# Kernel optimization log

Measured on AMD Instinct MI355X. Metric: run time of the kernel, lower is better.

The kernel has to match this reference:

```python
import jax, jax.numpy as jnp
import numpy as np

B, S, D = 4, 4096, 2048      # batch, seq, model_dim
E = 128                      # emb_dim (hardcoded in module)
H = 128                      # head_dim
TAU = 0.4                    # self.T
BASE = 3.0                   # self.base (gumbel-sigmoid offset)
LN_EPS = 1e-5


def setup_inputs() -> dict:
    key = jax.random.key(0)
    k_x, k_wr, k_wd, k_g = jax.random.split(key, 4)
    x = jax.random.normal(k_x, (B, S, D), dtype=jnp.float32)
    # torch nn.Linear stores weight as [out_features, in_features]
    W_router = jax.random.normal(k_wr, (E, D), dtype=jnp.float32) / np.sqrt(D)
    W_decoder = jax.random.normal(k_wd, (H, E), dtype=jnp.float32) / np.sqrt(E)
    ln_gamma = jnp.ones((E,), dtype=jnp.float32)
    ln_beta = jnp.zeros((E,), dtype=jnp.float32)
    rnn_state = jnp.zeros((E,), dtype=jnp.float32)  # registered buffer, zeros
    # torch: gumbels = -Exp(1).log()  -> standard Gumbel(0,1) noise
    u = jax.random.uniform(k_g, (B, S, H), dtype=jnp.float32, minval=1e-20, maxval=1.0)
    gumbel_noise = -jnp.log(-jnp.log(u))
    return {
        "x": x, "W_router": W_router, "W_decoder": W_decoder,
        "ln_gamma": ln_gamma, "ln_beta": ln_beta, "rnn_state": rnn_state,
        "gumbel_noise": gumbel_noise, "top_k": 32,
    }


def reference(x, W_router, W_decoder, ln_gamma, ln_beta, rnn_state, gumbel_noise, top_k):
    # router linear (no bias): [B,S,D] @ [D,E] -> [B,S,E]
    out = jnp.einsum("bsd,ed->bse", x, W_router)
    full_emb = rnn_state + out
    # LayerNorm over emb dim (biased variance, as torch LayerNorm)
    mu = full_emb.mean(-1, keepdims=True)
    var = full_emb.var(-1, keepdims=True)
    h = (full_emb - mu) / jnp.sqrt(var + LN_EPS) * ln_gamma + ln_beta
    # decoder linear after exact GELU: [B,S,E] @ [E,H] -> [B,S,H]
    logits = jnp.einsum("bse,he->bsh", jax.nn.gelu(h, approximate=False), W_decoder)
    # gumbel-sigmoid (soft): sigmoid((logits + gumbel + offset)/tau)
    binary_approx = jax.nn.sigmoid((logits + gumbel_noise + BASE) / TAU)
    # hard_sample: straight-through round
    binary = jax.lax.stop_gradient(jnp.round(binary_approx) - binary_approx) + binary_approx
    # top-k mask over head_dim
    _, topk_idx = jax.lax.top_k(binary_approx, top_k)            # [B,S,top_k]
    topk_mask = jax.nn.one_hot(topk_idx, H, dtype=binary_approx.dtype).sum(-2)  # [B,S,H]
    cnt = binary.sum(-1, keepdims=True)
    binary = jnp.where(cnt > top_k, topk_mask, binary)
    # fallback: if a token selects nothing, pick argmax of soft scores
    zero_mask = binary.sum(-1, keepdims=True) == 0
    fallback = jax.nn.one_hot(jnp.argmax(binary_approx, axis=-1), H, dtype=binary_approx.dtype)
    binary = jnp.where(zero_mask, fallback, binary)
    binary = binary.reshape(B, S, -1, H)  # [B,S,1,H]
    return binary, binary_approx
```

## Files before the change

### kernel.cpp

```cpp
#include <hip/hip_runtime.h>
#include <math.h>

#define NTOK   16384
#define DDIM   2048
#define EDIM   128
#define HDIM   128
#define TOKT   64
#define KC     32
#define NIT    32

typedef __attribute__((ext_vector_type(8))) _Float16 half8;
typedef __attribute__((ext_vector_type(4))) float    f32x4;

__device__ __forceinline__ int swz(int t, int e) {
  return t * EDIM + ((e & 96) | ((e ^ t) & 31));
}

__device__ __forceinline__ void cvt8(const float4& a, const float4& b,
                                     half8& h, half8& l) {
#pragma unroll
  for (int m = 0; m < 4; ++m) {
    const float v = (&a.x)[m];
    const _Float16 hv = (_Float16)v;
    h[m] = hv; l[m] = (_Float16)((v - (float)hv) * 2048.0f);
  }
#pragma unroll
  for (int m = 0; m < 4; ++m) {
    const float v = (&b.x)[m];
    const _Float16 hv = (_Float16)v;
    h[m + 4] = hv; l[m + 4] = (_Float16)((v - (float)hv) * 2048.0f);
  }
}

__global__ __launch_bounds__(256)
void conv_w(const float* __restrict__ Wr,
            _Float16* __restrict__ wh, _Float16* __restrict__ wl) {
  const int idx  = (int)blockIdx.x * 256 + (int)threadIdx.x;
  const int lane = idx & 63;
  const int ks   = (idx >> 6) & 63;
  const int nt   = idx >> 12;
  const int n    = nt * 16 + (lane & 15);
  const int k0   = ks * 32 + (lane >> 4) * 8;
  half8 h, l;
#pragma unroll
  for (int j = 0; j < 8; ++j) {
    const float w = Wr[(size_t)n * DDIM + k0 + j] * 32.0f;
    const _Float16 hh = (_Float16)w;
    h[j] = hh;
    l[j] = (_Float16)((w - (float)hh) * 2048.0f);
  }
  *(half8*)(wh + (size_t)idx * 8) = h;
  *(half8*)(wl + (size_t)idx * 8) = l;
}

__global__ __launch_bounds__(512, 2)
void fused_router(const float* __restrict__ x,
                  const _Float16* __restrict__ wsh,
                  const _Float16* __restrict__ wsl,
                  const float* __restrict__ Wd,
                  const float* __restrict__ gamma,
                  const float* __restrict__ beta,
                  const float* __restrict__ rnn,
                  const float* __restrict__ gum,
                  float* __restrict__ outb,
                  float* __restrict__ outa) {
  __shared__ char smraw[65536];
  _Float16* const xs = (_Float16*)smraw;
  float* const A  = (float*)smraw;
  float* const G4 = (float*)(smraw + 32768);

  const int tid  = (int)threadIdx.x;
  const int wv   = __builtin_amdgcn_readfirstlane(tid >> 6);
  const int lane = tid & 63;
  const int t0   = (int)blockIdx.x * TOKT;

  const int mw   = wv & 1;
  const int nw   = (wv >> 1) & 1;
  const int kw   = wv >> 2;
  const int quad = lane >> 4;
  const int col  = lane & 15;

  const int abase = (kw * 4 + mw * 2) * 1024 + lane * 8;

  const int skw   = tid >> 8;
  const int smt   = (tid >> 6) & 3;
  const int slane = tid & 63;
  const int woff  = (skw * 4 + smt) * 1024 + slane * 8;
  const float* xg = x + (size_t)(t0 + smt * 16 + (slane & 15)) * DDIM
                      + skw * 1024 + (slane >> 4) * 8;

  const size_t wbase = (size_t)(nw * 4) * 32768 + (size_t)kw * 16384 + lane * 8;

  f32x4 hh[2][4], cr[2][4];
#pragma unroll
  for (int mi = 0; mi < 2; ++mi)
#pragma unroll
    for (int ni = 0; ni < 4; ++ni) { hh[mi][ni] = (f32x4){0,0,0,0}; cr[mi][ni] = (f32x4){0,0,0,0}; }

  half8 bh[2][4], bl[2][4];

#pragma unroll
  for (int j = 0; j < 4; ++j) {
    bh[0][j] = *(const half8*)(wsh + wbase + (size_t)j * 32768);
    bl[0][j] = *(const half8*)(wsl + wbase + (size_t)j * 32768);
  }
  {
    const float4 a  = *(const float4*)xg;
    const float4 b2 = *(const float4*)(xg + 4);
    half8 h, l; cvt8(a, b2, h, l);
    *(half8*)&xs[woff] = h;
    *(half8*)&xs[woff + 512] = l;
  }

  auto body = [&](int i, int pb) {
    __syncthreads();
    const int ab = pb ? 8192 + abase : abase;
    const half8 ah0 = *(const half8*)&xs[ab];
    const half8 al0 = *(const half8*)&xs[ab + 512];
    const half8 ah1 = *(const half8*)&xs[ab + 1024];
    const half8 al1 = *(const half8*)&xs[ab + 1536];
    const int np = pb ^ 1;
    float4 pxa, pxb;
    if (i + 1 < NIT) {
      const size_t wo = wbase + (size_t)(i + 1) * 512;
#pragma unroll
      for (int j = 0; j < 4; ++j) {
        bh[np][j] = *(const half8*)(wsh + wo + (size_t)j * 32768);
        bl[np][j] = *(const half8*)(wsl + wo + (size_t)j * 32768);
      }
      pxa = *(const float4*)(xg + (i + 1) * KC);
      pxb = *(const float4*)(xg + (i + 1) * KC + 4);
    }
#pragma unroll
    for (int j = 0; j < 4; ++j) {
      hh[0][j] = __builtin_amdgcn_mfma_f32_16x16x32_f16(ah0, bh[pb][j], hh[0][j], 0, 0, 0);
      cr[0][j] = __builtin_amdgcn_mfma_f32_16x16x32_f16(ah0, bl[pb][j], cr[0][j], 0, 0, 0);
      cr[0][j] = __builtin_amdgcn_mfma_f32_16x16x32_f16(al0, bh[pb][j], cr[0][j], 0, 0, 0);
      hh[1][j] = __builtin_amdgcn_mfma_f32_16x16x32_f16(ah1, bh[pb][j], hh[1][j], 0, 0, 0);
      cr[1][j] = __builtin_amdgcn_mfma_f32_16x16x32_f16(ah1, bl[pb][j], cr[1][j], 0, 0, 0);
      cr[1][j] = __builtin_amdgcn_mfma_f32_16x16x32_f16(al1, bh[pb][j], cr[1][j], 0, 0, 0);
    }
    if (i + 1 < NIT) {
      half8 h, l; cvt8(pxa, pxb, h, l);
      *(half8*)&xs[np * 8192 + woff] = h;
      *(half8*)&xs[np * 8192 + woff + 512] = l;
    }
  };
  for (int ii = 0; ii < NIT; ii += 2) { body(ii, 0); body(ii + 1, 1); }
  __syncthreads();

  if (kw == 0) {
#pragma unroll
    for (int mi = 0; mi < 2; ++mi)
#pragma unroll
      for (int ni = 0; ni < 4; ++ni)
#pragma unroll
        for (int r = 0; r < 4; ++r) {
          const int t = (mw * 2 + mi) * 16 + quad * 4 + r;
          const int e = (nw * 4 + ni) * 16 + col;
          A[swz(t, e)] = hh[mi][ni][r] * (1.0f / 32.0f)
                       + cr[mi][ni][r] * (1.0f / 65536.0f);
        }
  }
  __syncthreads();
  if (kw == 1) {
    float rv[4];
#pragma unroll
    for (int ni = 0; ni < 4; ++ni) rv[ni] = rnn[(nw * 4 + ni) * 16 + col];
#pragma unroll
    for (int mi = 0; mi < 2; ++mi)
#pragma unroll
      for (int ni = 0; ni < 4; ++ni)
#pragma unroll
        for (int r = 0; r < 4; ++r) {
          const int t = (mw * 2 + mi) * 16 + quad * 4 + r;
          const int e = (nw * 4 + ni) * 16 + col;
          A[swz(t, e)] += hh[mi][ni][r] * (1.0f / 32.0f)
                        + cr[mi][ni][r] * (1.0f / 65536.0f) + rv[ni];
        }
  }
  __syncthreads();

  {
    const float gm0 = gamma[lane], gm1 = gamma[lane + 64];
    const float bt0 = beta[lane],  bt1 = beta[lane + 64];
    for (int tt = wv * 8; tt < wv * 8 + 8; ++tt) {
      const float v0 = A[swz(tt, lane)];
      const float v1 = A[swz(tt, lane + 64)];
      float s = v0 + v1;
#pragma unroll
      for (int m = 32; m; m >>= 1) s += __shfl_xor(s, m);
      const float mu = s * (1.0f / 128.0f);
      const float d0 = v0 - mu, d1 = v1 - mu;
      float q = d0 * d0 + d1 * d1;
#pragma unroll
      for (int m = 32; m; m >>= 1) q += __shfl_xor(q, m);
      const float rstd = 1.0f / sqrtf(q * (1.0f / 128.0f) + 1e-5f);
      const float h0v = d0 * rstd * gm0 + bt0;
      const float h1v = d1 * rstd * gm1 + bt1;
      const float g0 = 0.5f * h0v * (1.0f + erff(h0v * 0.70710678118654752f));
      const float g1 = 0.5f * h1v * (1.0f + erff(h1v * 0.70710678118654752f));
      const int e0a = lane, e1a = lane + 64;
      G4[(tt * 32 + (((e0a >> 2) ^ (tt & 31)))) * 4 + (e0a & 3)] = g0;
      G4[(tt * 32 + (((e1a >> 2) ^ (tt & 31)))) * 4 + (e1a & 3)] = g1;
    }
  }
  __syncthreads();

  {
    const int rbase = wv * 16;
    float acc2[16];
#pragma unroll
    for (int j = 0; j < 16; ++j) acc2[j] = 0.0f;
    const float4* wd4 = (const float4*)(Wd + (size_t)rbase * EDIM);
#pragma unroll 2
    for (int kg = 0; kg < EDIM / 4; ++kg) {
      const float4 gv = *(const float4*)&G4[(lane * 32 + (kg ^ (lane & 31))) * 4];
#pragma unroll
      for (int j = 0; j < 16; ++j) {
        const float4 w = wd4[(size_t)j * (EDIM / 4) + kg];
        acc2[j] = fmaf(gv.x, w.x,
                  fmaf(gv.y, w.y,
                  fmaf(gv.z, w.z,
                  fmaf(gv.w, w.w, acc2[j]))));
      }
    }
#pragma unroll
    for (int j = 0; j < 16; ++j) A[swz(lane, rbase + j)] = acc2[j];
  }
  __syncthreads();

  for (int tt = wv * 8; tt < wv * 8 + 8; ++tt) {
    const size_t T = (size_t)(t0 + tt);
    const float l0 = A[swz(tt, lane)];
    const float l1 = A[swz(tt, lane + 64)];
    const float gn0 = gum[T * HDIM + lane];
    const float gn1 = gum[T * HDIM + lane + 64];
    const float z0 = (l0 + gn0 + 3.0f) * 2.5f;
    const float z1 = (l1 + gn1 + 3.0f) * 2.5f;
    const float ba0 = 1.0f / (1.0f + expf(-z0));
    const float ba1 = 1.0f / (1.0f + expf(-z1));
    const unsigned ub0 = __float_as_uint(ba0);
    const unsigned ub1 = __float_as_uint(ba1);
    const int r0 = ba0 > 0.5f;
    const int r1 = ba1 > 0.5f;
    const int cnt = __popcll(__ballot(r0)) + __popcll(__ballot(r1));
    float bin0, bin1;
    if (cnt > 32) {
      unsigned v = 0u;
#pragma unroll
      for (int b = 29; b >= 0; --b) {
        const unsigned cand = v | (1u << b);
        const int cc = __popcll(__ballot(ub0 >= cand)) + __popcll(__ballot(ub1 >= cand));
        if (cc >= 32) v = cand;
      }
      const int cgt = __popcll(__ballot(ub0 > v)) + __popcll(__ballot(ub1 > v));
      const int r = 32 - cgt;
      const unsigned long long t0b = __ballot(ub0 == v);
      const unsigned long long t1b = __ballot(ub1 == v);
      const int n0 = __popcll(t0b);
      const unsigned long long mlt = (1ull << lane) - 1ull;
      const int rk0 = __popcll(t0b & mlt);
      const int rk1 = n0 + __popcll(t1b & mlt);
      bin0 = (ub0 > v || (ub0 == v && rk0 < r)) ? 1.0f : 0.0f;
      bin1 = (ub1 > v || (ub1 == v && rk1 < r)) ? 1.0f : 0.0f;
    } else if (cnt == 0) {
      float m = fmaxf(ba0, ba1);
#pragma unroll
      for (int mm = 32; mm; mm >>= 1) m = fmaxf(m, __shfl_xor(m, mm));
      const unsigned long long e0b = __ballot(ba0 == m);
      const unsigned long long e1b = __ballot(ba1 == m);
      const int hstar = e0b ? (__ffsll((unsigned long long)e0b) - 1)
                            : (64 + __ffsll((unsigned long long)e1b) - 1);
      bin0 = (lane == hstar) ? 1.0f : 0.0f;
      bin1 = (lane + 64 == hstar) ? 1.0f : 0.0f;
    } else {
      bin0 = r0 ? 1.0f : 0.0f;
      bin1 = r1 ? 1.0f : 0.0f;
    }
    outb[T * HDIM + lane]      = bin0;
    outb[T * HDIM + lane + 64] = bin1;
    outa[T * HDIM + lane]      = ba0;
    outa[T * HDIM + lane + 64] = ba1;
  }
}

extern "C" void kernel_launch(void* const* d_in, const int* in_sizes, int n_in,
                              void* d_out, int out_size, void* d_ws, size_t ws_size,
                              hipStream_t stream) {
  (void)in_sizes; (void)n_in; (void)ws_size; (void)out_size;
  const float* x   = (const float*)d_in[0];
  const float* Wr  = (const float*)d_in[1];
  const float* Wd  = (const float*)d_in[2];
  const float* gm  = (const float*)d_in[3];
  const float* bt  = (const float*)d_in[4];
  const float* rnn = (const float*)d_in[5];
  const float* gum = (const float*)d_in[6];
  float* outb = (float*)d_out;
  float* outa = outb + (size_t)NTOK * HDIM;

  _Float16* wh = (_Float16*)d_ws;
  _Float16* wl = wh + (size_t)EDIM * DDIM;

  conv_w<<<dim3(128), dim3(256), 0, stream>>>(Wr, wh, wl);
  fused_router<<<dim3(NTOK / TOKT), dim3(512), 0, stream>>>(
      x, wh, wl, Wd, gm, bt, rnn, gum, outb, outa);
}
```

Baseline: 281.3 us.

## Switch router GEMM to 32x32x16 MFMA with full-K per wave and larger K rounds

Restructures the split-fp16 router GEMM to use 32x32x16 MFMA tiles. Each of 8 waves now owns one 32x32 output tile over the full K range, where before the waves split K in two and reduced through LDS. Each barrier round now stages 128 K-columns instead of 32, with an XOR-swizzled LDS layout, and the weight preconversion kernel is reordered to match the new fragment layout. This cuts barrier count and the cross-wave reduction, at the cost of longer per-wave MFMA chains and unbuffered weight loads from global memory inside the inner loop. A barrier is also added before the decoder results overwrite the shared buffer.

```diff
diff --git a/kernel.cpp b/kernel.cpp
--- a/kernel.cpp
+++ b/kernel.cpp
@@ -6,11 +6,14 @@
 #define EDIM   128
 #define HDIM   128
 #define TOKT   64
-#define KC     32
-#define NIT    32
-
-typedef __attribute__((ext_vector_type(8))) _Float16 half8;
-typedef __attribute__((ext_vector_type(4))) float    f32x4;
+#define NRND   16
+#define KRND   128
+
+typedef __attribute__((ext_vector_type(8)))  _Float16 half8;
+typedef __attribute__((ext_vector_type(4)))  float    f32x4;
+typedef __attribute__((ext_vector_type(16))) float    f32x16;
+
+#define MFMA32 __builtin_amdgcn_mfma_f32_32x32x16_f16
 
 __device__ __forceinline__ int swz(int t, int e) {
   return t * EDIM + ((e & 96) | ((e ^ t) & 31));
@@ -37,10 +40,10 @@
             _Float16* __restrict__ wh, _Float16* __restrict__ wl) {
   const int idx  = (int)blockIdx.x * 256 + (int)threadIdx.x;
   const int lane = idx & 63;
-  const int ks   = (idx >> 6) & 63;
-  const int nt   = idx >> 12;
-  const int n    = nt * 16 + (lane & 15);
-  const int k0   = ks * 32 + (lane >> 4) * 8;
+  const int ks   = (idx >> 6) & 127;
+  const int nt   = idx >> 13;
+  const int n    = nt * 32 + (lane & 31);
+  const int k0   = ks * 16 + (lane >> 5) * 8;
   half8 h, l;
 #pragma unroll
   for (int j = 0; j < 8; ++j) {
@@ -65,7 +68,7 @@
                   float* __restrict__ outb,
                   float* __restrict__ outa) {
   __shared__ char smraw[65536];
-  _Float16* const xs = (_Float16*)smraw;
+  char* const sm = smraw;
   float* const A  = (float*)smraw;
   float* const G4 = (float*)(smraw + 32768);
 
@@ -74,110 +77,85 @@
   const int lane = tid & 63;
   const int t0   = (int)blockIdx.x * TOKT;
 
-  const int mw   = wv & 1;
-  const int nw   = (wv >> 1) & 1;
-  const int kw   = wv >> 2;
-  const int quad = lane >> 4;
-  const int col  = lane & 15;
-
-  const int abase = (kw * 4 + mw * 2) * 1024 + lane * 8;
-
-  const int skw   = tid >> 8;
-  const int smt   = (tid >> 6) & 3;
-  const int slane = tid & 63;
-  const int woff  = (skw * 4 + smt) * 1024 + slane * 8;
-  const float* xg = x + (size_t)(t0 + smt * 16 + (slane & 15)) * DDIM
-                      + skw * 1024 + (slane >> 4) * 8;
-
-  const size_t wbase = (size_t)(nw * 4) * 32768 + (size_t)kw * 16384 + lane * 8;
-
-  f32x4 hh[2][4], cr[2][4];
-#pragma unroll
-  for (int mi = 0; mi < 2; ++mi)
-#pragma unroll
-    for (int ni = 0; ni < 4; ++ni) { hh[mi][ni] = (f32x4){0,0,0,0}; cr[mi][ni] = (f32x4){0,0,0,0}; }
-
-  half8 bh[2][4], bl[2][4];
-
-#pragma unroll
-  for (int j = 0; j < 4; ++j) {
-    bh[0][j] = *(const half8*)(wsh + wbase + (size_t)j * 32768);
-    bl[0][j] = *(const half8*)(wsl + wbase + (size_t)j * 32768);
-  }
-  {
-    const float4 a  = *(const float4*)xg;
-    const float4 b2 = *(const float4*)(xg + 4);
-    half8 h, l; cvt8(a, b2, h, l);
-    *(half8*)&xs[woff] = h;
-    *(half8*)&xs[woff + 512] = l;
-  }
-
-  auto body = [&](int i, int pb) {
+  const int mt = wv >> 2;
+  const int nt = wv & 3;
+
+  const int s_tok = (tid & 7) + ((tid >> 6) << 3);
+  const int s_s   = (tid >> 3) & 7;
+  const int s_row = s_tok & 31;
+  const int s_mt  = s_tok >> 5;
+  const float* xg = x + (size_t)(t0 + s_tok) * DDIM + s_s * 16;
+  const int wbase = (s_s * 2 + s_mt) * 2048;
+  const int widx0 = (((0 * 32 + s_row) ^ s_s) * 16);
+  const int widx1 = (((1 * 32 + s_row) ^ s_s) * 16);
+
+  const size_t wbf = (size_t)nt * 65536 + (size_t)lane * 8;
+
+  f32x16 hh, cr;
+#pragma unroll
+  for (int g = 0; g < 16; ++g) { hh[g] = 0.0f; cr[g] = 0.0f; }
+
+  {
+    const float4 a0 = *(const float4*)(xg + 0);
+    const float4 a1 = *(const float4*)(xg + 4);
+    const float4 a2 = *(const float4*)(xg + 8);
+    const float4 a3 = *(const float4*)(xg + 12);
+    half8 h0, l0, h1, l1;
+    cvt8(a0, a1, h0, l0);
+    cvt8(a2, a3, h1, l1);
+    char* dst = sm;
+    *(half8*)(dst + wbase + widx0)        = h0;
+    *(half8*)(dst + wbase + 1024 + widx0) = l0;
+    *(half8*)(dst + wbase + widx1)        = h1;
+    *(half8*)(dst + wbase + 1024 + widx1) = l1;
+  }
+
+  for (int r = 0; r < NRND; ++r) {
     __syncthreads();
-    const int ab = pb ? 8192 + abase : abase;
-    const half8 ah0 = *(const half8*)&xs[ab];
-    const half8 al0 = *(const half8*)&xs[ab + 512];
-    const half8 ah1 = *(const half8*)&xs[ab + 1024];
-    const half8 al1 = *(const half8*)&xs[ab + 1536];
-    const int np = pb ^ 1;
-    float4 pxa, pxb;
-    if (i + 1 < NIT) {
-      const size_t wo = wbase + (size_t)(i + 1) * 512;
-#pragma unroll
-      for (int j = 0; j < 4; ++j) {
-        bh[np][j] = *(const half8*)(wsh + wo + (size_t)j * 32768);
-        bl[np][j] = *(const half8*)(wsl + wo + (size_t)j * 32768);
-      }
-      pxa = *(const float4*)(xg + (i + 1) * KC);
-      pxb = *(const float4*)(xg + (i + 1) * KC + 4);
-    }
-#pragma unroll
-    for (int j = 0; j < 4; ++j) {
-      hh[0][j] = __builtin_amdgcn_mfma_f32_16x16x32_f16(ah0, bh[pb][j], hh[0][j], 0, 0, 0);
-      cr[0][j] = __builtin_amdgcn_mfma_f32_16x16x32_f16(ah0, bl[pb][j], cr[0][j], 0, 0, 0);
-      cr[0][j] = __builtin_amdgcn_mfma_f32_16x16x32_f16(al0, bh[pb][j], cr[0][j], 0, 0, 0);
-      hh[1][j] = __builtin_amdgcn_mfma_f32_16x16x32_f16(ah1, bh[pb][j], hh[1][j], 0, 0, 0);
-      cr[1][j] = __builtin_amdgcn_mfma_f32_16x16x32_f16(ah1, bl[pb][j], cr[1][j], 0, 0, 0);
-      cr[1][j] = __builtin_amdgcn_mfma_f32_16x16x32_f16(al1, bh[pb][j], cr[1][j], 0, 0, 0);
-    }
-    if (i + 1 < NIT) {
-      half8 h, l; cvt8(pxa, pxb, h, l);
-      *(half8*)&xs[np * 8192 + woff] = h;
-      *(half8*)&xs[np * 8192 + woff + 512] = l;
-    }
-  };
-  for (int ii = 0; ii < NIT; ii += 2) { body(ii, 0); body(ii + 1, 1); }
-  __syncthreads();
-
-  if (kw == 0) {
-#pragma unroll
-    for (int mi = 0; mi < 2; ++mi)
-#pragma unroll
-      for (int ni = 0; ni < 4; ++ni)
-#pragma unroll
-        for (int r = 0; r < 4; ++r) {
-          const int t = (mw * 2 + mi) * 16 + quad * 4 + r;
-          const int e = (nw * 4 + ni) * 16 + col;
-          A[swz(t, e)] = hh[mi][ni][r] * (1.0f / 32.0f)
-                       + cr[mi][ni][r] * (1.0f / 65536.0f);
-        }
-  }
-  __syncthreads();
-  if (kw == 1) {
-    float rv[4];
-#pragma unroll
-    for (int ni = 0; ni < 4; ++ni) rv[ni] = rnn[(nw * 4 + ni) * 16 + col];
-#pragma unroll
-    for (int mi = 0; mi < 2; ++mi)
-#pragma unroll
-      for (int ni = 0; ni < 4; ++ni)
-#pragma unroll
-        for (int r = 0; r < 4; ++r) {
-          const int t = (mw * 2 + mi) * 16 + quad * 4 + r;
-          const int e = (nw * 4 + ni) * 16 + col;
-          A[swz(t, e)] += hh[mi][ni][r] * (1.0f / 32.0f)
-                        + cr[mi][ni][r] * (1.0f / 65536.0f) + rv[ni];
-        }
+    float4 p0, p1, p2, p3;
+    if (r + 1 < NRND) {
+      const float* xn = xg + (r + 1) * KRND;
+      p0 = *(const float4*)(xn + 0);
+      p1 = *(const float4*)(xn + 4);
+      p2 = *(const float4*)(xn + 8);
+      p3 = *(const float4*)(xn + 12);
+    }
+    const char* bb = sm + (r & 1) * 32768;
+#pragma unroll
+    for (int s = 0; s < 8; ++s) {
+      const int fb = (s * 2 + mt) * 2048;
+      const int ai = (lane ^ s) * 16;
+      const half8 ah = *(const half8*)(bb + fb + ai);
+      const half8 al = *(const half8*)(bb + fb + 1024 + ai);
+      const size_t wo = wbf + (size_t)(r * 8 + s) * 512;
+      const half8 bh = *(const half8*)(wsh + wo);
+      const half8 bl = *(const half8*)(wsl + wo);
+      hh = MFMA32(ah, bh, hh, 0, 0, 0);
+      cr = MFMA32(ah, bl, cr, 0, 0, 0);
+      cr = MFMA32(al, bh, cr, 0, 0, 0);
+    }
+    if (r + 1 < NRND) {
+      half8 h0, l0, h1, l1;
+      cvt8(p0, p1, h0, l0);
+      cvt8(p2, p3, h1, l1);
+      char* dst = sm + ((r + 1) & 1) * 32768;
+      *(half8*)(dst + wbase + widx0)        = h0;
+      *(half8*)(dst + wbase + 1024 + widx0) = l0;
+      *(half8*)(dst + wbase + widx1)        = h1;
+      *(half8*)(dst + wbase + 1024 + widx1) = l1;
+    }
+  }
+  __syncthreads();
+
+  {
+    const int e = nt * 32 + (lane & 31);
+    const float rv = rnn[e];
+#pragma unroll
+    for (int g = 0; g < 16; ++g) {
+      const int row = (g & 3) + 8 * (g >> 2) + 4 * (lane >> 5);
+      A[swz(mt * 32 + row, e)] =
+          hh[g] * (1.0f / 32.0f) + cr[g] * (1.0f / 65536.0f) + rv;
+    }
   }
   __syncthreads();
 
@@ -225,6 +203,7 @@
                   fmaf(gv.w, w.w, acc2[j]))));
       }
     }
+    __syncthreads();
 #pragma unroll
     for (int j = 0; j < 16; ++j) A[swz(lane, rbase + j)] = acc2[j];
   }
```

Result: no change. 280.6 us (-0.3%).
